# Performance work log

Measured on AMD Instinct MI355X. Metric: run time of the kernel, lower is better.

Reference implementation:

```python
import jax, jax.numpy as jnp
import numpy as np

B, F, D = 1024, 256, 64  # batch, featureNumb, featureDim


def setup_inputs() -> dict:
    key = jax.random.key(0)
    k1, k2, k3, k4 = jax.random.split(key, 4)
    feature = jax.random.normal(k1, (B, F, D), dtype=jnp.float32)
    indicator = jax.random.normal(k2, (F, D), dtype=jnp.float32)
    # QKVTransformV2(n, D, D): n stacked DxD linear maps of the indicator
    W_qk = jax.random.normal(k3, (2, D, D), dtype=jnp.float32) / np.float32(np.sqrt(D))
    W_qkv = jax.random.normal(k4, (3, D, D), dtype=jnp.float32) / np.float32(np.sqrt(D))
    return {"feature": feature, "indicator": indicator, "W_qk": W_qk, "W_qkv": W_qkv}


def reference(feature, indicator, W_qk, W_qkv):
    d = indicator.shape[-1]
    scale = jnp.asarray(1.0 / np.sqrt(d), feature.dtype)

    # --- gate branch: QKTrans + DotWeight + LTE (straight-through hard threshold) ---
    trans = jnp.einsum('fd,nde->nfe', indicator, W_qk)            # [2,F,D]
    gate_logits = jnp.einsum('id,jd->ij', trans[0], trans[1]) * scale  # [F,F]
    gate = (gate_logits > 0).astype(feature.dtype)                # LTE forward: hard 0/1 gate

    # --- QKV branch, fused form of the rank-1 outer products ---
    # Original: QKV_outer[t,i,j] = qkv[t,i] (x) qkv[t,j]  (DxD rank-1)
    #           input[b,t,i,j,:] = feature[b,i] @ QKV_outer[t,i,j]
    #                            = (feature[b,i] . qkv[t,i]) * qkv[t,j]
    qkv = jnp.einsum('fd,nde->nfe', indicator, W_qkv)             # [3,F,D]
    s = jnp.einsum('bfd,nfd->nbf', feature, qkv)                  # s[t,b,i] = feature[b,i].qkv[t,i]

    # score[b,i,j] = input[b,0,i,j,:] . input[b,1,j,i,:]
    #              = s[0,b,i] * s[1,b,j] * (qkv[1,i] . qkv[0,j])
    cross = jnp.einsum('id,jd->ij', qkv[1], qkv[0])               # [F,F]
    score = s[0][:, :, None] * s[1][:, None, :] * cross[None]     # [B,F,F]
    scoreHat = score * gate[None]                                 # [B,F,F]

    # output[b,i,:] = sum_j scoreHat[b,i,j] * value[b,i,j,:]
    #               = s[2,b,i] * sum_j scoreHat[b,i,j] * qkv[2,j,:]
    out = s[2][:, :, None] * jnp.einsum('bij,jd->bid', scoreHat, qkv[2])  # [B,F,D]
    return out
```

## Files before the change

kernel.cpp:

```cpp
#include <hip/hip_runtime.h>
#include <stdint.h>

#define B 1024
#define F 256
#define D 64

typedef __attribute__((ext_vector_type(8))) short short8;
typedef __attribute__((ext_vector_type(4))) float f32x4;

__device__ __forceinline__ short f2bf(float f) {
    unsigned u = __builtin_bit_cast(unsigned, f);
    u += 0x7fff + ((u >> 16) & 1);
    return (short)(u >> 16);
}
__device__ __forceinline__ float bf2f(short s) {
    unsigned u = ((unsigned)(unsigned short)s) << 16;
    return __builtin_bit_cast(float, u);
}
__device__ __forceinline__ unsigned pk_bf16(float a, float b) {
    unsigned ua = __builtin_bit_cast(unsigned, a) + 0x8000u;
    unsigned ub = __builtin_bit_cast(unsigned, b) + 0x8000u;
    return __builtin_amdgcn_perm(ub, ua, 0x07060302u);
}

__device__ __forceinline__ float dot4(float4 a, float4 b) {
    return a.x * b.x + a.y * b.y + a.z * b.z + a.w * b.w;
}


__global__ void precompute_trans(const float* __restrict__ indicator,
                                 const float* __restrict__ W_qk,
                                 const float* __restrict__ W_qkv,
                                 float* __restrict__ trans,
                                 float* __restrict__ qkv) {
    int idx = blockIdx.x * blockDim.x + threadIdx.x;
    int n   = idx / (F * D);
    int rem = idx - n * (F * D);
    int f   = rem / D;
    int e   = rem - f * D;
    const float* W = (n < 2) ? (W_qk + n * D * D) : (W_qkv + (n - 2) * D * D);
    const float* ind = indicator + f * D;
    float acc = 0.f;
#pragma unroll 8
    for (int d = 0; d < D; ++d) acc += ind[d] * W[d * D + e];
    if (n < 2) trans[n * F * D + f * D + e] = acc;
    else       qkv[(n - 2) * F * D + f * D + e] = acc;
}

__global__ __launch_bounds__(256, 8) void s_and_Mt(const float* __restrict__ feature,
                                                   const float* __restrict__ trans,
                                                   const float* __restrict__ qkv,
                                                   float* __restrict__ gS,
                                                   short* __restrict__ s1S,
                                                   short* __restrict__ At,
                                                   short* __restrict__ q2K) {
    int blk = blockIdx.x;
    int tid = threadIdx.x;
    if (blk < B) {
        int b0   = (blk >> 1) * 2;
        int half = blk & 1;
        int rg   = tid >> 4;
        int l    = tid & 15;
#pragma unroll 2
        for (int p = 0; p < 8; ++p) {
            int f = half * 128 + p * 16 + rg;
            float4 fv0 = ((const float4*)(feature + ((size_t)(b0 * F + f)) * D))[l];
            float4 fv1 = ((const float4*)(feature + ((size_t)((b0 + 1) * F + f)) * D))[l];
            float4 q0 = ((const float4*)(qkv + f * D))[l];
            float4 q1 = ((const float4*)(qkv + F * D + f * D))[l];
            float4 q2 = ((const float4*)(qkv + 2 * F * D + f * D))[l];
            float a00 = dot4(fv0, q0);
            float a01 = dot4(fv0, q1);
            float a02 = dot4(fv0, q2);
            float a10 = dot4(fv1, q0);
            float a11 = dot4(fv1, q1);
            float a12 = dot4(fv1, q2);
#pragma unroll
            for (int m = 1; m < 16; m <<= 1) {
                a00 += __shfl_xor(a00, m, 64);
                a01 += __shfl_xor(a01, m, 64);
                a02 += __shfl_xor(a02, m, 64);
                a10 += __shfl_xor(a10, m, 64);
                a11 += __shfl_xor(a11, m, 64);
                a12 += __shfl_xor(a12, m, 64);
            }
            if (l == 0) {
                gS[b0 * F + f]        = a00 * a02;
                gS[(b0 + 1) * F + f]  = a10 * a12;
                s1S[b0 * F + f]       = f2bf(a01);
                s1S[(b0 + 1) * F + f] = f2bf(a11);
            }
        }
    } else {
        int j = blk - B;
        int i = tid;
        const float4* t0 = (const float4*)(trans + i * D);
        const float4* t1 = (const float4*)(trans + F * D + j * D);
        const float4* q1 = (const float4*)(qkv + F * D + i * D);
        const float4* q0 = (const float4*)(qkv + j * D);
        float d0 = 0.f, d1 = 0.f;
#pragma unroll 2
        for (int k = 0; k < D / 4; ++k) {
            float4 a = t0[k], b = t1[k], c = q1[k], e = q0[k];
            d0 += dot4(a, b);
            d1 += dot4(c, e);
        }
        float v = (d0 > 0.f) ? d1 : 0.f;
        At[((j >> 5) * F + i) * 32 + (j & 31)] = f2bf(v);
        if (j < D) {
            int p = (j & 3) * 16 + (j >> 2);
            q2K[((i >> 5) * D + p) * 32 + (i & 31)] = f2bf(qkv[2 * F * D + i * D + j]);
        }
    }
}

__global__ __launch_bounds__(512, 4) void gemm_out(const short* __restrict__ At,
                                                   const short* __restrict__ q2K,
                                                   const float* __restrict__ gS,
                                                   const short* __restrict__ s1S,
                                                   float* __restrict__ out) {
    int it  = blockIdx.x & 3;
    int bg  = blockIdx.x >> 2;
    int tid = threadIdx.x;

    __shared__ __align__(16) short AtL[8 * 64 * 32];
    __shared__ __align__(16) short q2L[8 * 64 * 32];

    {
        const float4* Ag = (const float4*)At;
        const float4* Qg = (const float4*)q2K;
        float4* Al = (float4*)AtL;
        float4* Ql = (float4*)q2L;
#pragma unroll
        for (int v = tid; v < 2048; v += 512) {
            int jt = v >> 8, k = v & 255;
            Al[v] = Ag[jt * 1024 + it * 256 + k];
        }
#pragma unroll
        for (int v = tid; v < 2048; v += 512) Ql[v] = Qg[v];
    }
    __syncthreads();

    int w    = tid >> 6;
    int lane = tid & 63;
    int l16  = lane & 15;
    int lq   = lane >> 4;
    int kq   = lq * 8;
    int b    = bg * 8 + w;

    const short* s1b = s1S + b * F;

    f32x4 acc[4][4];
#pragma unroll
    for (int mt = 0; mt < 4; ++mt)
#pragma unroll
        for (int nt = 0; nt < 4; ++nt) acc[mt][nt] = (f32x4){0.f, 0.f, 0.f, 0.f};

    for (int jt = 0; jt < F / 32; ++jt) {
        short8 sv = *(const short8*)(s1b + jt * 32 + kq);
        float sf[8];
#pragma unroll
        for (int e = 0; e < 8; ++e) sf[e] = bf2f(sv[e]);

        short8 bfr[4];
#pragma unroll
        for (int nt = 0; nt < 4; ++nt) {
            int d = nt * 16 + l16;
            short8 qv = *(const short8*)(q2L + (jt * 64 + d) * 32 + kq);
            int4 packed;
            packed.x = pk_bf16(bf2f(qv[0]) * sf[0], bf2f(qv[1]) * sf[1]);
            packed.y = pk_bf16(bf2f(qv[2]) * sf[2], bf2f(qv[3]) * sf[3]);
            packed.z = pk_bf16(bf2f(qv[4]) * sf[4], bf2f(qv[5]) * sf[5]);
            packed.w = pk_bf16(bf2f(qv[6]) * sf[6], bf2f(qv[7]) * sf[7]);
            bfr[nt] = __builtin_bit_cast(short8, packed);
        }
#pragma unroll
        for (int mt = 0; mt < 4; ++mt) {
            short8 af = *(const short8*)(AtL + (jt * 64 + mt * 16 + l16) * 32 + kq);
#pragma unroll
            for (int nt = 0; nt < 4; ++nt)
                acc[mt][nt] = __builtin_amdgcn_mfma_f32_16x16x32_bf16(
                    af, bfr[nt], acc[mt][nt], 0, 0, 0);
        }
    }

    const float4* g4 = (const float4*)(gS + b * F + it * 64);
#pragma unroll
    for (int mt = 0; mt < 4; ++mt) {
        float4 gg = g4[mt * 4 + lq];
        float* obase = out + ((size_t)(b * F + it * 64 + mt * 16 + lq * 4)) * D + l16 * 4;
        float4 v0 = {gg.x * acc[mt][0][0], gg.x * acc[mt][1][0],
                     gg.x * acc[mt][2][0], gg.x * acc[mt][3][0]};
        float4 v1 = {gg.y * acc[mt][0][1], gg.y * acc[mt][1][1],
                     gg.y * acc[mt][2][1], gg.y * acc[mt][3][1]};
        float4 v2 = {gg.z * acc[mt][0][2], gg.z * acc[mt][1][2],
                     gg.z * acc[mt][2][2], gg.z * acc[mt][3][2]};
        float4 v3 = {gg.w * acc[mt][0][3], gg.w * acc[mt][1][3],
                     gg.w * acc[mt][2][3], gg.w * acc[mt][3][3]};
        *(float4*)(obase + 0 * D) = v0;
        *(float4*)(obase + 1 * D) = v1;
        *(float4*)(obase + 2 * D) = v2;
        *(float4*)(obase + 3 * D) = v3;
    }
}

extern "C" void kernel_launch(void* const* d_in, const int* in_sizes, int n_in,
                              void* d_out, int out_size, void* d_ws, size_t ws_size,
                              hipStream_t stream) {
    const float* feature   = (const float*)d_in[0];
    const float* indicator = (const float*)d_in[1];
    const float* W_qk      = (const float*)d_in[2];
    const float* W_qkv     = (const float*)d_in[3];
    float* out = (float*)d_out;

    float* ws    = (float*)d_ws;
    float* trans = ws;
    float* qkv   = trans + 2 * F * D;
    float* gS    = qkv + 3 * F * D;
    short* At    = (short*)(gS + B * F);
    short* q2K   = At + F * F;
    short* s1S   = q2K + (F / 32) * D * 32;

    hipLaunchKernelGGL(precompute_trans, dim3((5 * F * D) / 256), dim3(256), 0,
                       stream, indicator, W_qk, W_qkv, trans, qkv);
    hipLaunchKernelGGL(s_and_Mt, dim3(B + F), dim3(256), 0, stream,
                       feature, trans, qkv, gS, s1S, At, q2K);
    hipLaunchKernelGGL(gemm_out, dim3((B / 8) * 4), dim3(512), 0, stream,
                       At, q2K, gS, s1S, out);
}
```

Measured before the change: 142.6 us.

## Fuse per-batch s computation into GEMM kernel; split gate matrix into own kernel

The per-batch dot products (gS, s1) are now computed inside the GEMM kernel and kept in shared memory, so the gS/s1S global round trip goes away. The masked cross matrix At moves to a small separate kernel. Each block now handles two batches, with 8 waves split into 2 batches by 4 row tiles. At is read directly from global (L2) instead of being staged in LDS. The risks are a smaller grid of 512 blocks, a serial phase before the MFMA loop, and uncached At reads from global.

```diff
diff --git a/kernel.cpp b/kernel.cpp
--- a/kernel.cpp
+++ b/kernel.cpp
@@ -47,23 +47,57 @@
     else       qkv[(n - 2) * F * D + f * D + e] = acc;
 }
 
-__global__ __launch_bounds__(256, 8) void s_and_Mt(const float* __restrict__ feature,
-                                                   const float* __restrict__ trans,
+__global__ __launch_bounds__(256) void compute_Mt(const float* __restrict__ trans,
+                                                  const float* __restrict__ qkv,
+                                                  short* __restrict__ At,
+                                                  short* __restrict__ q2K) {
+    int j = blockIdx.x;
+    int i = threadIdx.x;
+    const float4* t0 = (const float4*)(trans + i * D);
+    const float4* t1 = (const float4*)(trans + F * D + j * D);
+    const float4* q1 = (const float4*)(qkv + F * D + i * D);
+    const float4* q0 = (const float4*)(qkv + j * D);
+    float d0 = 0.f, d1 = 0.f;
+#pragma unroll
+    for (int k = 0; k < D / 4; ++k) {
+        float4 a = t0[k], b = t1[k], c = q1[k], e = q0[k];
+        d0 += dot4(a, b);
+        d1 += dot4(c, e);
+    }
+    float v = (d0 > 0.f) ? d1 : 0.f;
+    At[((j >> 5) * F + i) * 32 + (j & 31)] = f2bf(v);
+    if (j < D) {
+        int p = (j & 3) * 16 + (j >> 2);
+        q2K[((i >> 5) * D + p) * 32 + (i & 31)] = f2bf(qkv[2 * F * D + i * D + j]);
+    }
+}
+
+__global__ __launch_bounds__(512, 4) void fused_sg(const float* __restrict__ feature,
                                                    const float* __restrict__ qkv,
-                                                   float* __restrict__ gS,
-                                                   short* __restrict__ s1S,
-                                                   short* __restrict__ At,
-                                                   short* __restrict__ q2K) {
-    int blk = blockIdx.x;
+                                                   const short* __restrict__ At,
+                                                   const short* __restrict__ q2K,
+                                                   float* __restrict__ out) {
+    int bp  = blockIdx.x;
+    int b0  = bp * 2;
     int tid = threadIdx.x;
-    if (blk < B) {
-        int b0   = (blk >> 1) * 2;
-        int half = blk & 1;
-        int rg   = tid >> 4;
-        int l    = tid & 15;
+
+    __shared__ __align__(16) short q2L[8 * 64 * 32];
+    __shared__ __align__(16) short s1L[2 * F];
+    __shared__ __align__(16) float gL[2 * F];
+
+    {
+        const float4* Qg = (const float4*)q2K;
+        float4* Ql = (float4*)q2L;
+#pragma unroll
+        for (int v = tid; v < 2048; v += 512) Ql[v] = Qg[v];
+    }
+
+    {
+        int rg = tid >> 4;
+        int l  = tid & 15;
 #pragma unroll 2
         for (int p = 0; p < 8; ++p) {
-            int f = half * 128 + p * 16 + rg;
+            int f = p * 32 + rg;
             float4 fv0 = ((const float4*)(feature + ((size_t)(b0 * F + f)) * D))[l];
             float4 fv1 = ((const float4*)(feature + ((size_t)((b0 + 1) * F + f)) * D))[l];
             float4 q0 = ((const float4*)(qkv + f * D))[l];
@@ -85,59 +119,12 @@
                 a12 += __shfl_xor(a12, m, 64);
             }
             if (l == 0) {
-                gS[b0 * F + f]        = a00 * a02;
-                gS[(b0 + 1) * F + f]  = a10 * a12;
-                s1S[b0 * F + f]       = f2bf(a01);
-                s1S[(b0 + 1) * F + f] = f2bf(a11);
+                gL[f]      = a00 * a02;
+                gL[F + f]  = a10 * a12;
+                s1L[f]     = f2bf(a01);
+                s1L[F + f] = f2bf(a11);
             }
         }
-    } else {
-        int j = blk - B;
-        int i = tid;
-        const float4* t0 = (const float4*)(trans + i * D);
-        const float4* t1 = (const float4*)(trans + F * D + j * D);
-        const float4* q1 = (const float4*)(qkv + F * D + i * D);
-        const float4* q0 = (const float4*)(qkv + j * D);
-        float d0 = 0.f, d1 = 0.f;
-#pragma unroll 2
-        for (int k = 0; k < D / 4; ++k) {
-            float4 a = t0[k], b = t1[k], c = q1[k], e = q0[k];
-            d0 += dot4(a, b);
-            d1 += dot4(c, e);
-        }
-        float v = (d0 > 0.f) ? d1 : 0.f;
-        At[((j >> 5) * F + i) * 32 + (j & 31)] = f2bf(v);
-        if (j < D) {
-            int p = (j & 3) * 16 + (j >> 2);
-            q2K[((i >> 5) * D + p) * 32 + (i & 31)] = f2bf(qkv[2 * F * D + i * D + j]);
-        }
-    }
-}
-
-__global__ __launch_bounds__(512, 4) void gemm_out(const short* __restrict__ At,
-                                                   const short* __restrict__ q2K,
-                                                   const float* __restrict__ gS,
-                                                   const short* __restrict__ s1S,
-                                                   float* __restrict__ out) {
-    int it  = blockIdx.x & 3;
-    int bg  = blockIdx.x >> 2;
-    int tid = threadIdx.x;
-
-    __shared__ __align__(16) short AtL[8 * 64 * 32];
-    __shared__ __align__(16) short q2L[8 * 64 * 32];
-
-    {
-        const float4* Ag = (const float4*)At;
-        const float4* Qg = (const float4*)q2K;
-        float4* Al = (float4*)AtL;
-        float4* Ql = (float4*)q2L;
-#pragma unroll
-        for (int v = tid; v < 2048; v += 512) {
-            int jt = v >> 8, k = v & 255;
-            Al[v] = Ag[jt * 1024 + it * 256 + k];
-        }
-#pragma unroll
-        for (int v = tid; v < 2048; v += 512) Ql[v] = Qg[v];
     }
     __syncthreads();
 
@@ -146,9 +133,9 @@
     int l16  = lane & 15;
     int lq   = lane >> 4;
     int kq   = lq * 8;
-    int b    = bg * 8 + w;
-
-    const short* s1b = s1S + b * F;
+    int wc   = w & 1;
+    int it   = w >> 1;
+    int b    = b0 + wc;
 
     f32x4 acc[4][4];
 #pragma unroll
@@ -157,7 +144,7 @@
         for (int nt = 0; nt < 4; ++nt) acc[mt][nt] = (f32x4){0.f, 0.f, 0.f, 0.f};
 
     for (int jt = 0; jt < F / 32; ++jt) {
-        short8 sv = *(const short8*)(s1b + jt * 32 + kq);
+        short8 sv = *(const short8*)(s1L + wc * F + jt * 32 + kq);
         float sf[8];
 #pragma unroll
         for (int e = 0; e < 8; ++e) sf[e] = bf2f(sv[e]);
@@ -176,7 +163,7 @@
         }
 #pragma unroll
         for (int mt = 0; mt < 4; ++mt) {
-            short8 af = *(const short8*)(AtL + (jt * 64 + mt * 16 + l16) * 32 + kq);
+            short8 af = *(const short8*)(At + ((size_t)jt * F + it * 64 + mt * 16 + l16) * 32 + kq);
 #pragma unroll
             for (int nt = 0; nt < 4; ++nt)
                 acc[mt][nt] = __builtin_amdgcn_mfma_f32_16x16x32_bf16(
@@ -184,7 +171,7 @@
         }
     }
 
-    const float4* g4 = (const float4*)(gS + b * F + it * 64);
+    const float4* g4 = (const float4*)(gL + wc * F + it * 64);
 #pragma unroll
     for (int mt = 0; mt < 4; ++mt) {
         float4 gg = g4[mt * 4 + lq];
@@ -216,15 +203,12 @@
     float* ws    = (float*)d_ws;
     float* trans = ws;
     float* qkv   = trans + 2 * F * D;
-    float* gS    = qkv + 3 * F * D;
-    short* At    = (short*)(gS + B * F);
+    short* At    = (short*)(qkv + 3 * F * D);
     short* q2K   = At + F * F;
-    short* s1S   = q2K + (F / 32) * D * 32;
 
     hipLaunchKernelGGL(precompute_trans, dim3((5 * F * D) / 256), dim3(256), 0,
                        stream, indicator, W_qk, W_qkv, trans, qkv);
-    hipLaunchKernelGGL(s_and_Mt, dim3(B + F), dim3(256), 0, stream,
-                       feature, trans, qkv, gS, s1S, At, q2K);
-    hipLaunchKernelGGL(gemm_out, dim3((B / 8) * 4), dim3(512), 0, stream,
-                       At, q2K, gS, s1S, out);
-}
+    hipLaunchKernelGGL(compute_Mt, dim3(F), dim3(256), 0, stream, trans, qkv, At, q2K);
+    hipLaunchKernelGGL(fused_sg, dim3(B / 2), dim3(512), 0, stream,
+                       feature, qkv, At, q2K, out);
+}
```

Measured after the change: 144.9 us. Within noise of the previous version (+1.7%).
